# Kernel tuning notes

Hardware: AMD Instinct MI355X
Metric: run time of the kernel (lower is better)

The kernel has to match this reference:

```python
import math
import jax, jax.numpy as jnp
import numpy as np

IN_CH = 64
NUM_ANCHOR = 4
MAP_H, MAP_W = 96, 96
BATCH = 8
BN_EPS = 1e-5


def _conv2d(x, w, b, padding, dilation):
    # x: [B,C,H,W], w: [O,I,kh,kw] (OIHW)
    y = jax.lax.conv_general_dilated(
        x, w, window_strides=(1, 1),
        padding=((padding, padding), (padding, padding)),
        rhs_dilation=(dilation, dilation),
        dimension_numbers=('NCHW', 'OIHW', 'NCHW'))
    return y + b[None, :, None, None]


def _bn(x, gamma, beta, mean, var):
    scale = gamma / jnp.sqrt(var + BN_EPS)
    return x * scale[None, :, None, None] + (beta - mean * scale)[None, :, None, None]


def setup_inputs() -> dict:
    key = jax.random.key(0)
    ks = jax.random.split(key, 12)
    # cyclic channel-shift permutation matrices, one per anchor pass
    eye = np.eye(IN_CH, dtype=np.float32)
    shift = IN_CH // (2 * NUM_ANCHOR)
    perms = np.stack([eye[np.roll(np.arange(IN_CH), i * shift)] for i in range(2 * NUM_ANCHOR)])
    w_std = 1.0 / math.sqrt(IN_CH * 9)
    return {
        'x': jax.random.normal(ks[0], (BATCH, IN_CH, MAP_H, MAP_W), dtype=jnp.float32),
        'perms': jnp.asarray(perms),
        'dcn_w': jax.random.normal(ks[1], (IN_CH, IN_CH, 3, 3), dtype=jnp.float32) * w_std,
        'dcn_b': jax.random.normal(ks[2], (IN_CH,), dtype=jnp.float32) * 0.01,
        'conv2_w': jax.random.normal(ks[3], (IN_CH, IN_CH, 3, 3), dtype=jnp.float32) * w_std,
        'conv2_b': jax.random.normal(ks[4], (IN_CH,), dtype=jnp.float32) * 0.01,
        'conv3_w': jax.random.normal(ks[5], (IN_CH, IN_CH, 3, 3), dtype=jnp.float32) * w_std,
        'conv3_b': jax.random.normal(ks[6], (IN_CH,), dtype=jnp.float32) * 0.01,
        'bn_gamma': jax.random.uniform(ks[7], (3, IN_CH), dtype=jnp.float32, minval=0.5, maxval=1.5),
        'bn_beta': jax.random.normal(ks[8], (3, IN_CH), dtype=jnp.float32) * 0.1,
        'bn_mean': jax.random.normal(ks[9], (3, IN_CH), dtype=jnp.float32) * 0.1,
        'bn_var': jax.random.uniform(ks[10], (3, IN_CH), dtype=jnp.float32, minval=0.5, maxval=1.5),
    }


def reference(x, perms, dcn_w, dcn_b, conv2_w, conv2_b, conv3_w, conv3_b,
              bn_gamma, bn_beta, bn_mean, bn_var):
    h = x.shape[2]
    pad = math.ceil(h / (2 ** 1.5 + 2))  # 20 for h=96

    def conv_stack(o):
        # DCN at init (zero offsets) == plain 3x3 conv, pad=1
        o = jax.nn.relu(_bn(_conv2d(o, dcn_w, dcn_b, 1, 1), bn_gamma[0], bn_beta[0], bn_mean[0], bn_var[0]))
        o = jax.nn.relu(_bn(_conv2d(o, conv2_w, conv2_b, 2, 2), bn_gamma[1], bn_beta[1], bn_mean[1], bn_var[1]))
        o = jax.nn.relu(_bn(_conv2d(o, conv3_w, conv3_b, 2, 2), bn_gamma[2], bn_beta[2], bn_mean[2], bn_var[2]))
        return o

    outs = []
    for i in range(2 * NUM_ANCHOR):  # fixed small structural loop
        o = jnp.einsum('mn,bnhw->bmhw', perms[i], x)  # channel permutation
        if i % 2 != 0:
            o = jnp.pad(o, ((0, 0), (0, 0), (pad, pad), (pad, pad)))
        o = jnp.rot90(o, k=i % 4, axes=(-2, -1))   # ccw rotate
        o = conv_stack(o)
        o = jnp.rot90(o, k=(-i) % 4, axes=(-2, -1))  # cw rotate back
        if i % 2 != 0:
            H, W = o.shape[-2], o.shape[-1]
            sh, sw = (H - MAP_H) // 2, (W - MAP_W) // 2
            o = o[..., sh:sh + MAP_H, sw:sw + MAP_W]  # center crop
        outs.append(o)
    out_tensor = jnp.concatenate(outs, axis=1)  # [B, 8*C, H, W]
    out = jnp.max(out_tensor, axis=1, keepdims=True)
    # branch_name == 'midpoint', orientational_anchor=False -> clamped sigmoid
    return jnp.clip(jax.nn.sigmoid(out), 1e-4, 1.0 - 1e-4)
```

## Files before the change

kernel.cpp:

```cpp
#include <hip/hip_runtime.h>
#include <math.h>

#define B 8
#define C 64
#define HW 96
#define NWV 36864

typedef __attribute__((ext_vector_type(8)))  short short8;
typedef __attribute__((ext_vector_type(16))) float floatx16;

__device__ __forceinline__ unsigned short f2bf(float f) {
    unsigned int u = __float_as_uint(f);
    unsigned int r = (u + 0x7fffu + ((u >> 16) & 1u)) >> 16;
    return (unsigned short)r;
}

__device__ __forceinline__ void rotmap(int k, int ta, int tb, int& sa, int& sb) {
    switch (k) {
        case 0: sa = ta;     sb = tb;     break;
        case 1: sa = 2 - tb; sb = ta;     break;
        case 2: sa = 2 - ta; sb = 2 - tb; break;
        default: sa = tb;    sb = 2 - ta; break;
    }
}

__global__ void prep_w(const float* __restrict__ dcn_w, const float* __restrict__ c2w,
                       const float* __restrict__ c3w,
                       const float* __restrict__ gamma, const float* __restrict__ var_,
                       unsigned short* __restrict__ Wall) {
    int idx = blockIdx.x * 256 + threadIdx.x;
    if (idx >= 16 * NWV) return;
    int v = idx / NWV, rem = idx % NWV;
    int tap  = rem >> 12;
    int w12  = rem & 4095;
    int ks   = w12 >> 10;
    int cf   = (w12 >> 9) & 1;
    int lane = (w12 >> 3) & 63;
    int j    = w12 & 7;
    int co = cf * 32 + (lane & 31);
    int ci = ks * 16 + (lane >> 5) * 8 + j;
    int ta = tap / 3, tb = tap % 3;
    const float* src; int k, srcci, l;
    if (v < 8)       { k = v & 3;  srcci = (ci + 8 * v) & 63; src = dcn_w; l = 0; }
    else if (v < 12) { k = v - 8;  srcci = ci; src = c2w; l = 1; }
    else             { k = v - 12; srcci = ci; src = c3w; l = 2; }
    int sa, sb; rotmap(k, ta, tb, sa, sb);
    float s = gamma[l * 64 + co] * rsqrtf(var_[l * 64 + co] + 1e-5f);
    Wall[idx] = f2bf(src[((co * 64 + srcci) * 3 + sa) * 3 + sb] * s);
}

__global__ void prep_bias(const float* __restrict__ dcn_b, const float* __restrict__ c2b,
                          const float* __restrict__ c3b,
                          const float* __restrict__ gamma, const float* __restrict__ beta,
                          const float* __restrict__ mean, const float* __restrict__ var_,
                          float* __restrict__ biasg) {
    int t = threadIdx.x;
    if (t < 192) {
        int l = t >> 6, c = t & 63;
        const float* cb = (l == 0) ? dcn_b : ((l == 1) ? c2b : c3b);
        float s = gamma[l * 64 + c] * rsqrtf(var_[l * 64 + c] + 1e-5f);
        biasg[t] = cb[c] * s + beta[l * 64 + c] - mean[l * 64 + c] * s;
    }
}

__global__ __launch_bounds__(256) void prep_x(const float* __restrict__ in,
                                              unsigned short* __restrict__ out) {
    __shared__ float row[64 * 97];
    int by = blockIdx.x;
    int b = by / 96, y = by % 96;
    int t = threadIdx.x;
    for (int e = t; e < 6144; e += 256) {
        int c = e / 96, x = e - c * 96;
        row[c * 97 + x] = in[(((size_t)(b * 64 + c) * 96 + y) * 96) + x];
    }
    __syncthreads();
    for (int e = t; e < 6144; e += 256) {
        int x = e >> 6, c = e & 63;
        out[(((size_t)(b * 96 + y) * 96 + x) << 6) + c] = f2bf(row[c * 97 + x]);
    }
}

__global__ __launch_bounds__(256) void border_clear(unsigned short* __restrict__ buf1) {
    int idx = blockIdx.y;
    int br = (idx >> 3) * 2, b = idx & 7;
    int z = br * 8 + b;
    int i = blockIdx.x * 32 + (threadIdx.x >> 3);
    int g = threadIdx.x & 7;
    int r, c;
    if (i < 416)      { r = i / 104;              c = i % 104; }
    else if (i < 832) { int j = i - 416; r = 100 + j / 104; c = j % 104; }
    else              { int j = i - 832; r = 4 + (j >> 3); int c8 = j & 7;
                        c = (c8 < 4) ? c8 : 92 + c8; }
    uint4 zero = make_uint4(0u, 0u, 0u, 0u);
    *(uint4*)(buf1 + (size_t)z * (104 * 104 * 64) + ((size_t)(r * 104 + c) << 6) + (g << 3)) = zero;
}

__global__ __launch_bounds__(256, 2) void conv1_k(
    const unsigned short* __restrict__ xhwc, unsigned short* __restrict__ buf1,
    const unsigned short* __restrict__ Wall, const float* __restrict__ biasg) {

    __shared__ __align__(16) unsigned short xt[10 * 34 * 64];

    int z = blockIdx.z, br = z >> 3, b = z & 7, odd = br & 1;
    int fy0 = blockIdx.y * 8, fx0 = blockIdx.x * 32;
    int t = threadIdx.x, lane = t & 63, wv = t >> 6;
    int n = lane & 31, kq = lane >> 5;

    const unsigned short* xb = xhwc + ((size_t)b * 96 * 96 << 6);
    const short8* Ag = (const short8*)(Wall + (size_t)br * NWV);

    for (int e = t; e < 2720; e += 256) {
        int p = e >> 3, g = e & 7;
        int yy = p / 34, xx = p - yy * 34;
        int gy = fy0 - 5 + yy, gx = fx0 - 5 + xx;
        uint4 v = make_uint4(0u, 0u, 0u, 0u);
        if ((unsigned)gy < 96u && (unsigned)gx < 96u)
            v = *(const uint4*)(xb + ((size_t)(gy * 96 + gx) << 6) + (g << 3));
        *(uint4*)(xt + (p << 6) + ((g ^ (xx & 7)) << 3)) = v;
    }
    __syncthreads();

    floatx16 acc[2][2];
#pragma unroll
    for (int cf = 0; cf < 2; cf++)
#pragma unroll
        for (int pf = 0; pf < 2; pf++)
#pragma unroll
            for (int i = 0; i < 16; i++) acc[cf][pf][i] = 0.f;

#pragma unroll
    for (int ks = 0; ks < 4; ks++) {
#pragma unroll
        for (int tb = 0; tb < 3; tb++) {
            short8 a[3][2];
#pragma unroll
            for (int ta = 0; ta < 3; ta++)
#pragma unroll
                for (int cf = 0; cf < 2; cf++)
                    a[ta][cf] = Ag[(((ta * 3 + tb) * 4 + ks) * 2 + cf) * 64 + lane];
            int xx = n + tb;
            int g = ((ks * 2 + kq) ^ (xx & 7)) << 3;
            short8 bf[4];
#pragma unroll
            for (int rr = 0; rr < 4; rr++) {
                int p = (2 * wv + rr) * 34 + xx;
                bf[rr] = *(const short8*)(xt + (p << 6) + g);
            }
#pragma unroll
            for (int ta = 0; ta < 3; ta++)
#pragma unroll
                for (int pf = 0; pf < 2; pf++) {
                    int rr = pf + ta;
                    acc[0][pf] = __builtin_amdgcn_mfma_f32_32x32x16_bf16(a[ta][0], bf[rr], acc[0][pf], 0, 0, 0);
                    acc[1][pf] = __builtin_amdgcn_mfma_f32_32x32x16_bf16(a[ta][1], bf[rr], acc[1][pf], 0, 0, 0);
                }
        }
    }

    float4 bv[2][4];
#pragma unroll
    for (int cf = 0; cf < 2; cf++)
#pragma unroll
        for (int rb = 0; rb < 4; rb++)
            bv[cf][rb] = *(const float4*)(biasg + 32 * cf + 8 * rb + 4 * kq);

    __syncthreads();
#pragma unroll
    for (int pf = 0; pf < 2; pf++) {
        int pq = (2 * wv + pf) * 32 + n;
        int key = (pq & 7) << 1;
#pragma unroll
        for (int cf = 0; cf < 2; cf++)
#pragma unroll
            for (int rb = 0; rb < 4; rb++) {
                int u = kq + 2 * rb + 8 * cf;
                float v0 = fmaxf(acc[cf][pf][rb * 4 + 0] + bv[cf][rb].x, 0.f);
                float v1 = fmaxf(acc[cf][pf][rb * 4 + 1] + bv[cf][rb].y, 0.f);
                float v2 = fmaxf(acc[cf][pf][rb * 4 + 2] + bv[cf][rb].z, 0.f);
                float v3 = fmaxf(acc[cf][pf][rb * 4 + 3] + bv[cf][rb].w, 0.f);
                uint2 pk = make_uint2((unsigned)f2bf(v0) | ((unsigned)f2bf(v1) << 16),
                                      (unsigned)f2bf(v2) | ((unsigned)f2bf(v3) << 16));
                *(uint2*)((char*)xt + pq * 128 + ((u ^ key) << 3)) = pk;
            }
    }
    __syncthreads();

    unsigned short* fb = buf1 + (size_t)z * (104 * 104 * 64);
    int lo = odd ? 0 : 4, hi = odd ? 104 : 100;
    for (int e = t; e < 2048; e += 256) {
        int px = e >> 3, g = e & 7;
        int key = (px & 7) << 1;
        uint4 v = *(const uint4*)((const char*)xt + px * 128 + (((2 * g) ^ key) << 3));
        int lr = px >> 5, nn = px & 31;
        int f = fy0 + lr, fc = fx0 + nn;
        if (f >= lo && f < hi && fc >= lo && fc < hi)
            *(uint4*)(fb + ((size_t)(f * 104 + fc) << 6) + (g << 3)) = v;
    }
}

__global__ __launch_bounds__(512, 2) void conv23_k(
    const unsigned short* __restrict__ buf1, float* __restrict__ maxb,
    const unsigned short* __restrict__ Wall, const float* __restrict__ biasg) {

    __shared__ __align__(16) unsigned short c2out[768 * 64];
    __shared__ __align__(16) unsigned short xs[960 * 32];

    int z = blockIdx.z, br = z >> 3, odd = br & 1;
    int oy0 = blockIdx.y * 16, ox0 = blockIdx.x * 32;
    int t = threadIdx.x, lane = t & 63, wv = t >> 6;
    int n = lane & 31, kq = lane >> 5;

    const unsigned short* fb = buf1 + (size_t)z * (104 * 104 * 64);
    const short8* A2 = (const short8*)(Wall + (size_t)(8  + (br & 3)) * NWV);
    const short8* A3 = (const short8*)(Wall + (size_t)(12 + (br & 3)) * NWV);

    for (int e = t; e < 3840; e += 512) {
        int p = e >> 2, g = e & 3;
        int yy = p / 40, xx = p - yy * 40;
        uint4 v = *(const uint4*)(fb + ((size_t)((oy0 + yy) * 104 + ox0 + xx) << 6) + (g << 3));
        *(uint4*)(xs + (p << 5) + ((g ^ (xx & 3)) << 3)) = v;
    }
    __syncthreads();

    uint4 pfv[8];
#pragma unroll
    for (int k = 0; k < 8; k++) {
        int e = t + k * 512;
        if (e < 3840) {
            int p = e >> 2, g = e & 3;
            int yy = p / 40, xx = p - yy * 40;
            pfv[k] = *(const uint4*)(fb + ((size_t)((oy0 + yy) * 104 + ox0 + xx) << 6) + 32 + (g << 3));
        }
    }

    int q_[3], row2_[3], col2_[3];
#pragma unroll
    for (int jj = 0; jj < 3; jj++) {
        int q = 96 * wv + 32 * jj + n;
        q_[jj] = q;
        int qc = (q < 720) ? q : 719;
        int r2 = qc / 36;
        row2_[jj] = r2;
        col2_[jj] = qc - 36 * r2;
    }

    floatx16 acc2[3][2];
#pragma unroll
    for (int jj = 0; jj < 3; jj++)
#pragma unroll
        for (int cf = 0; cf < 2; cf++)
#pragma unroll
            for (int i = 0; i < 16; i++) acc2[jj][cf][i] = 0.f;

#pragma unroll
    for (int s = 0; s < 2; s++) {
        if (s == 1) {
            __syncthreads();
#pragma unroll
            for (int k = 0; k < 8; k++) {
                int e = t + k * 512;
                if (e < 3840) {
                    int p = e >> 2, g = e & 3;
                    int xx2 = p - (p / 40) * 40;
                    *(uint4*)(xs + (p << 5) + ((g ^ (xx2 & 3)) << 3)) = pfv[k];
                }
            }
            __syncthreads();
        }
#pragma unroll
        for (int kl = 0; kl < 2; kl++) {
            int ks = s * 2 + kl;
#pragma unroll
            for (int tb = 0; tb < 3; tb++) {
                short8 a[3][2];
#pragma unroll
                for (int ta = 0; ta < 3; ta++)
#pragma unroll
                    for (int cf = 0; cf < 2; cf++)
                        a[ta][cf] = A2[(((ta * 3 + tb) * 4 + ks) * 2 + cf) * 64 + lane];
#pragma unroll
                for (int jj = 0; jj < 3; jj++) {
                    int colx = col2_[jj] + 2 * tb;
                    int gsw = ((kl * 2 + kq) ^ (colx & 3)) << 3;
#pragma unroll
                    for (int ta = 0; ta < 3; ta++) {
                        int p = (row2_[jj] + 2 * ta) * 40 + colx;
                        short8 bfr = *(const short8*)(xs + (p << 5) + gsw);
                        acc2[jj][0] = __builtin_amdgcn_mfma_f32_32x32x16_bf16(a[ta][0], bfr, acc2[jj][0], 0, 0, 0);
                        acc2[jj][1] = __builtin_amdgcn_mfma_f32_32x32x16_bf16(a[ta][1], bfr, acc2[jj][1], 0, 0, 0);
                    }
                }
            }
        }
    }

    int rlo2 = (!odd && oy0 == 0)  ? 2  : 0;
    int rhi2 = (!odd && oy0 == 80) ? 18 : 20;
    int clo2 = (!odd && ox0 == 0)  ? 2  : 0;
    int chi2 = (!odd && ox0 == 64) ? 34 : 36;
    float4 bv2[2][4];
#pragma unroll
    for (int cf = 0; cf < 2; cf++)
#pragma unroll
        for (int rb = 0; rb < 4; rb++)
            bv2[cf][rb] = *(const float4*)(biasg + 64 + 32 * cf + 8 * rb + 4 * kq);

#pragma unroll
    for (int jj = 0; jj < 3; jj++) {
        if (q_[jj] < 720) {
            bool valid = (row2_[jj] >= rlo2) && (row2_[jj] < rhi2) &&
                         (col2_[jj] >= clo2) && (col2_[jj] < chi2);
            int key = col2_[jj] & 14;
#pragma unroll
            for (int cf = 0; cf < 2; cf++)
#pragma unroll
                for (int rb = 0; rb < 4; rb++) {
                    int u = kq + 2 * rb + 8 * cf;
                    float v0 = 0.f, v1 = 0.f, v2 = 0.f, v3 = 0.f;
                    if (valid) {
                        v0 = fmaxf(acc2[jj][cf][rb * 4 + 0] + bv2[cf][rb].x, 0.f);
                        v1 = fmaxf(acc2[jj][cf][rb * 4 + 1] + bv2[cf][rb].y, 0.f);
                        v2 = fmaxf(acc2[jj][cf][rb * 4 + 2] + bv2[cf][rb].z, 0.f);
                        v3 = fmaxf(acc2[jj][cf][rb * 4 + 3] + bv2[cf][rb].w, 0.f);
                    }
                    uint2 pk = make_uint2((unsigned)f2bf(v0) | ((unsigned)f2bf(v1) << 16),
                                          (unsigned)f2bf(v2) | ((unsigned)f2bf(v3) << 16));
                    *(uint2*)((char*)c2out + q_[jj] * 128 + ((u ^ key) << 3)) = pk;
                }
        }
    }
    __syncthreads();

    int r0 = 2 * wv;
    floatx16 acc3[2][2];
#pragma unroll
    for (int cf = 0; cf < 2; cf++)
#pragma unroll
        for (int pf = 0; pf < 2; pf++)
#pragma unroll
            for (int i = 0; i < 16; i++) acc3[cf][pf][i] = 0.f;

#pragma unroll
    for (int ks = 0; ks < 4; ks++) {
#pragma unroll
        for (int tb = 0; tb < 3; tb++) {
            short8 a[3][2];
#pragma unroll
            for (int ta = 0; ta < 3; ta++)
#pragma unroll
                for (int cf = 0; cf < 2; cf++)
                    a[ta][cf] = A3[(((ta * 3 + tb) * 4 + ks) * 2 + cf) * 64 + lane];
            int col = n + 2 * tb;
            int key = col & 14;
            int ublk = 2 * (ks * 2 + kq);
            short8 bf[6];
#pragma unroll
            for (int rr = 0; rr < 6; rr++) {
                int q = (r0 + rr) * 36 + col;
                bf[rr] = *(const short8*)((const char*)c2out + q * 128 + ((ublk ^ key) << 3));
            }
#pragma unroll
            for (int ta = 0; ta < 3; ta++)
#pragma unroll
                for (int pf = 0; pf < 2; pf++) {
                    int rr = pf + 2 * ta;
                    acc3[0][pf] = __builtin_amdgcn_mfma_f32_32x32x16_bf16(a[ta][0], bf[rr], acc3[0][pf], 0, 0, 0);
                    acc3[1][pf] = __builtin_amdgcn_mfma_f32_32x32x16_bf16(a[ta][1], bf[rr], acc3[1][pf], 0, 0, 0);
                }
        }
    }

    float4 bv3[2][4];
#pragma unroll
    for (int cf = 0; cf < 2; cf++)
#pragma unroll
        for (int rb = 0; rb < 4; rb++)
            bv3[cf][rb] = *(const float4*)(biasg + 128 + 32 * cf + 8 * rb + 4 * kq);

#pragma unroll
    for (int pf = 0; pf < 2; pf++) {
        float m = 0.f;
#pragma unroll
        for (int cf = 0; cf < 2; cf++)
#pragma unroll
            for (int rb = 0; rb < 4; rb++) {
                m = fmaxf(m, acc3[cf][pf][rb * 4 + 0] + bv3[cf][rb].x);
                m = fmaxf(m, acc3[cf][pf][rb * 4 + 1] + bv3[cf][rb].y);
                m = fmaxf(m, acc3[cf][pf][rb * 4 + 2] + bv3[cf][rb].z);
                m = fmaxf(m, acc3[cf][pf][rb * 4 + 3] + bv3[cf][rb].w);
            }
        m = fmaxf(m, 0.f);
        m = fmaxf(m, __shfl_xor(m, 32, 64));
        if (lane < 32)
            maxb[((size_t)z * 96 + oy0 + r0 + pf) * 96 + ox0 + n] = m;
    }
}

__global__ void final_k(const float* __restrict__ maxb, float* __restrict__ out) {
    int i = blockIdx.x * 256 + threadIdx.x;
    if (i < B * HW * HW) {
        int b = i / 9216, yx = i - b * 9216;
        float m = 0.f;
#pragma unroll
        for (int br = 0; br < 8; br++)
            m = fmaxf(m, maxb[((size_t)(br * 8 + b)) * 9216 + yx]);
        float v = 1.f / (1.f + expf(-m));
        out[i] = fminf(fmaxf(v, 1e-4f), 1.f - 1e-4f);
    }
}


extern "C" void kernel_launch(void* const* d_in, const int* in_sizes, int n_in,
                              void* d_out, int out_size, void* d_ws, size_t ws_size,
                              hipStream_t stream) {
    const float* x     = (const float*)d_in[0];
    const float* dcn_w = (const float*)d_in[2];
    const float* dcn_b = (const float*)d_in[3];
    const float* c2w   = (const float*)d_in[4];
    const float* c2b   = (const float*)d_in[5];
    const float* c3w   = (const float*)d_in[6];
    const float* c3b   = (const float*)d_in[7];
    const float* gamma = (const float*)d_in[8];
    const float* beta  = (const float*)d_in[9];
    const float* mean  = (const float*)d_in[10];
    const float* var_  = (const float*)d_in[11];

    char* ws = (char*)d_ws;
    unsigned short* Wall = (unsigned short*)ws;
    size_t off = (size_t)16 * NWV * 2;
    float* biasg = (float*)(ws + off);            off += 1024;
    float* maxb  = (float*)(ws + off);            off += (size_t)64 * 9216 * 4;
    unsigned short* xhwc = (unsigned short*)(ws + off); off += (size_t)B * 9216 * 64 * 2;
    unsigned short* buf1 = (unsigned short*)(ws + off);

    prep_w<<<(16 * NWV + 255) / 256, 256, 0, stream>>>(dcn_w, c2w, c3w, gamma, var_, Wall);
    prep_bias<<<1, 256, 0, stream>>>(dcn_b, c2b, c3b, gamma, beta, mean, var_, biasg);
    prep_x<<<B * 96, 256, 0, stream>>>(x, xhwc);
    border_clear<<<dim3(50, 32), 256, 0, stream>>>(buf1);

    dim3 g1(4, 13, 64);
    conv1_k<<<g1, 256, 0, stream>>>(xhwc, buf1, Wall, biasg);

    dim3 g23(3, 6, 64);
    conv23_k<<<g23, 512, 0, stream>>>(buf1, maxb, Wall, biasg);

    final_k<<<(B * HW * HW + 255) / 256, 256, 0, stream>>>(maxb, (float*)d_out);
}
```

Before: 310.5 us.

## Make conv23 persistent over 256 blocks with cross-tile prefetch

Replaces the 1152-block conv23 grid with 256 persistent blocks, each looping over a contiguous range of tiles. While conv3 runs on the current tile, the block prefetches the first channel half of the next tile's input into registers and writes it to shared memory afterwards. Bias loads are hoisted out of the loop. This hides global load latency and removes tail-wave imbalance, but adds register pressure and leaves 4-5 tiles per block, which may lower occupancy.

```diff
diff --git a/kernel.cpp b/kernel.cpp
--- a/kernel.cpp
+++ b/kernel.cpp
@@ -205,33 +205,20 @@
     __shared__ __align__(16) unsigned short c2out[768 * 64];
     __shared__ __align__(16) unsigned short xs[960 * 32];
 
-    int z = blockIdx.z, br = z >> 3, odd = br & 1;
-    int oy0 = blockIdx.y * 16, ox0 = blockIdx.x * 32;
     int t = threadIdx.x, lane = t & 63, wv = t >> 6;
     int n = lane & 31, kq = lane >> 5;
 
-    const unsigned short* fb = buf1 + (size_t)z * (104 * 104 * 64);
-    const short8* A2 = (const short8*)(Wall + (size_t)(8  + (br & 3)) * NWV);
-    const short8* A3 = (const short8*)(Wall + (size_t)(12 + (br & 3)) * NWV);
-
-    for (int e = t; e < 3840; e += 512) {
-        int p = e >> 2, g = e & 3;
-        int yy = p / 40, xx = p - yy * 40;
-        uint4 v = *(const uint4*)(fb + ((size_t)((oy0 + yy) * 104 + ox0 + xx) << 6) + (g << 3));
-        *(uint4*)(xs + (p << 5) + ((g ^ (xx & 3)) << 3)) = v;
-    }
-    __syncthreads();
-
-    uint4 pfv[8];
-#pragma unroll
-    for (int k = 0; k < 8; k++) {
-        int e = t + k * 512;
-        if (e < 3840) {
-            int p = e >> 2, g = e & 3;
-            int yy = p / 40, xx = p - yy * 40;
-            pfv[k] = *(const uint4*)(fb + ((size_t)((oy0 + yy) * 104 + ox0 + xx) << 6) + 32 + (g << 3));
-        }
-    }
+    int i0 = (blockIdx.x * 1152) >> 8;
+    int i1 = ((blockIdx.x + 1) * 1152) >> 8;
+
+    float4 bv2[2][4], bv3[2][4];
+#pragma unroll
+    for (int cf = 0; cf < 2; cf++)
+#pragma unroll
+        for (int rb = 0; rb < 4; rb++) {
+            bv2[cf][rb] = *(const float4*)(biasg + 64  + 32 * cf + 8 * rb + 4 * kq);
+            bv3[cf][rb] = *(const float4*)(biasg + 128 + 32 * cf + 8 * rb + 4 * kq);
+        }
 
     int q_[3], row2_[3], col2_[3];
 #pragma unroll
@@ -244,155 +231,206 @@
         col2_[jj] = qc - 36 * r2;
     }
 
-    floatx16 acc2[3][2];
-#pragma unroll
-    for (int jj = 0; jj < 3; jj++)
+    {
+        int z = i0 / 18, r = i0 - z * 18;
+        int oy0 = (r % 6) * 16, ox0 = (r / 6) * 32;
+        const unsigned short* fb = buf1 + (size_t)z * (104 * 104 * 64);
+        for (int e = t; e < 3840; e += 512) {
+            int p = e >> 2, g = e & 3;
+            int yy = p / 40, xx = p - yy * 40;
+            uint4 v = *(const uint4*)(fb + ((size_t)((oy0 + yy) * 104 + ox0 + xx) << 6) + (g << 3));
+            *(uint4*)(xs + (p << 5) + ((g ^ (xx & 3)) << 3)) = v;
+        }
+    }
+
+    for (int i = i0; i < i1; ++i) {
+        int z = i / 18, r = i - z * 18;
+        int br = z >> 3, odd = br & 1;
+        int oy0 = (r % 6) * 16, ox0 = (r / 6) * 32;
+        const unsigned short* fb = buf1 + (size_t)z * (104 * 104 * 64);
+        const short8* A2 = (const short8*)(Wall + (size_t)(8  + (br & 3)) * NWV);
+        const short8* A3 = (const short8*)(Wall + (size_t)(12 + (br & 3)) * NWV);
+
+        __syncthreads();
+
+        uint4 pfv[8];
+#pragma unroll
+        for (int k = 0; k < 8; k++) {
+            int e = t + k * 512;
+            if (e < 3840) {
+                int p = e >> 2, g = e & 3;
+                int yy = p / 40, xx = p - yy * 40;
+                pfv[k] = *(const uint4*)(fb + ((size_t)((oy0 + yy) * 104 + ox0 + xx) << 6) + 32 + (g << 3));
+            }
+        }
+
+        floatx16 acc2[3][2];
+#pragma unroll
+        for (int jj = 0; jj < 3; jj++)
+#pragma unroll
+            for (int cf = 0; cf < 2; cf++)
+#pragma unroll
+                for (int q = 0; q < 16; q++) acc2[jj][cf][q] = 0.f;
+
+#pragma unroll
+        for (int s = 0; s < 2; s++) {
+            if (s == 1) {
+                __syncthreads();
+#pragma unroll
+                for (int k = 0; k < 8; k++) {
+                    int e = t + k * 512;
+                    if (e < 3840) {
+                        int p = e >> 2, g = e & 3;
+                        int xx2 = p - (p / 40) * 40;
+                        *(uint4*)(xs + (p << 5) + ((g ^ (xx2 & 3)) << 3)) = pfv[k];
+                    }
+                }
+                __syncthreads();
+            }
+#pragma unroll
+            for (int kl = 0; kl < 2; kl++) {
+                int ks = s * 2 + kl;
+#pragma unroll
+                for (int tb = 0; tb < 3; tb++) {
+                    short8 a[3][2];
+#pragma unroll
+                    for (int ta = 0; ta < 3; ta++)
+#pragma unroll
+                        for (int cf = 0; cf < 2; cf++)
+                            a[ta][cf] = A2[(((ta * 3 + tb) * 4 + ks) * 2 + cf) * 64 + lane];
+#pragma unroll
+                    for (int jj = 0; jj < 3; jj++) {
+                        int colx = col2_[jj] + 2 * tb;
+                        int gsw = ((kl * 2 + kq) ^ (colx & 3)) << 3;
+#pragma unroll
+                        for (int ta = 0; ta < 3; ta++) {
+                            int p = (row2_[jj] + 2 * ta) * 40 + colx;
+                            short8 bfr = *(const short8*)(xs + (p << 5) + gsw);
+                            acc2[jj][0] = __builtin_amdgcn_mfma_f32_32x32x16_bf16(a[ta][0], bfr, acc2[jj][0], 0, 0, 0);
+                            acc2[jj][1] = __builtin_amdgcn_mfma_f32_32x32x16_bf16(a[ta][1], bfr, acc2[jj][1], 0, 0, 0);
+                        }
+                    }
+                }
+            }
+        }
+
+        int rlo2 = (!odd && oy0 == 0)  ? 2  : 0;
+        int rhi2 = (!odd && oy0 == 80) ? 18 : 20;
+        int clo2 = (!odd && ox0 == 0)  ? 2  : 0;
+        int chi2 = (!odd && ox0 == 64) ? 34 : 36;
+
+#pragma unroll
+        for (int jj = 0; jj < 3; jj++) {
+            if (q_[jj] < 720) {
+                bool valid = (row2_[jj] >= rlo2) && (row2_[jj] < rhi2) &&
+                             (col2_[jj] >= clo2) && (col2_[jj] < chi2);
+                int key = col2_[jj] & 14;
+#pragma unroll
+                for (int cf = 0; cf < 2; cf++)
+#pragma unroll
+                    for (int rb = 0; rb < 4; rb++) {
+                        int u = kq + 2 * rb + 8 * cf;
+                        float v0 = 0.f, v1 = 0.f, v2 = 0.f, v3 = 0.f;
+                        if (valid) {
+                            v0 = fmaxf(acc2[jj][cf][rb * 4 + 0] + bv2[cf][rb].x, 0.f);
+                            v1 = fmaxf(acc2[jj][cf][rb * 4 + 1] + bv2[cf][rb].y, 0.f);
+                            v2 = fmaxf(acc2[jj][cf][rb * 4 + 2] + bv2[cf][rb].z, 0.f);
+                            v3 = fmaxf(acc2[jj][cf][rb * 4 + 3] + bv2[cf][rb].w, 0.f);
+                        }
+                        uint2 pk = make_uint2((unsigned)f2bf(v0) | ((unsigned)f2bf(v1) << 16),
+                                              (unsigned)f2bf(v2) | ((unsigned)f2bf(v3) << 16));
+                        *(uint2*)((char*)c2out + q_[jj] * 128 + ((u ^ key) << 3)) = pk;
+                    }
+            }
+        }
+        __syncthreads();
+
+        bool have_next = (i + 1 < i1);
+        uint4 nfv[8];
+        if (have_next) {
+            int ni = i + 1;
+            int nz = ni / 18, nr = ni - nz * 18;
+            int noy0 = (nr % 6) * 16, nox0 = (nr / 6) * 32;
+            const unsigned short* nfb = buf1 + (size_t)nz * (104 * 104 * 64);
+#pragma unroll
+            for (int k = 0; k < 8; k++) {
+                int e = t + k * 512;
+                if (e < 3840) {
+                    int p = e >> 2, g = e & 3;
+                    int yy = p / 40, xx = p - yy * 40;
+                    nfv[k] = *(const uint4*)(nfb + ((size_t)((noy0 + yy) * 104 + nox0 + xx) << 6) + (g << 3));
+                }
+            }
+        }
+
+        int r0 = 2 * wv;
+        floatx16 acc3[2][2];
 #pragma unroll
         for (int cf = 0; cf < 2; cf++)
 #pragma unroll
-            for (int i = 0; i < 16; i++) acc2[jj][cf][i] = 0.f;
-
-#pragma unroll
-    for (int s = 0; s < 2; s++) {
-        if (s == 1) {
-            __syncthreads();
+            for (int pf = 0; pf < 2; pf++)
+#pragma unroll
+                for (int q = 0; q < 16; q++) acc3[cf][pf][q] = 0.f;
+
+#pragma unroll
+        for (int ks = 0; ks < 4; ks++) {
+#pragma unroll
+            for (int tb = 0; tb < 3; tb++) {
+                short8 a[3][2];
+#pragma unroll
+                for (int ta = 0; ta < 3; ta++)
+#pragma unroll
+                    for (int cf = 0; cf < 2; cf++)
+                        a[ta][cf] = A3[(((ta * 3 + tb) * 4 + ks) * 2 + cf) * 64 + lane];
+                int col = n + 2 * tb;
+                int key = col & 14;
+                int ublk = 2 * (ks * 2 + kq);
+                short8 bf[6];
+#pragma unroll
+                for (int rr = 0; rr < 6; rr++) {
+                    int q = (r0 + rr) * 36 + col;
+                    bf[rr] = *(const short8*)((const char*)c2out + q * 128 + ((ublk ^ key) << 3));
+                }
+#pragma unroll
+                for (int ta = 0; ta < 3; ta++)
+#pragma unroll
+                    for (int pf = 0; pf < 2; pf++) {
+                        int rr = pf + 2 * ta;
+                        acc3[0][pf] = __builtin_amdgcn_mfma_f32_32x32x16_bf16(a[ta][0], bf[rr], acc3[0][pf], 0, 0, 0);
+                        acc3[1][pf] = __builtin_amdgcn_mfma_f32_32x32x16_bf16(a[ta][1], bf[rr], acc3[1][pf], 0, 0, 0);
+                    }
+            }
+        }
+
+        if (have_next) {
 #pragma unroll
             for (int k = 0; k < 8; k++) {
                 int e = t + k * 512;
                 if (e < 3840) {
                     int p = e >> 2, g = e & 3;
                     int xx2 = p - (p / 40) * 40;
-                    *(uint4*)(xs + (p << 5) + ((g ^ (xx2 & 3)) << 3)) = pfv[k];
-                }
-            }
-            __syncthreads();
-        }
-#pragma unroll
-        for (int kl = 0; kl < 2; kl++) {
-            int ks = s * 2 + kl;
-#pragma unroll
-            for (int tb = 0; tb < 3; tb++) {
-                short8 a[3][2];
-#pragma unroll
-                for (int ta = 0; ta < 3; ta++)
-#pragma unroll
-                    for (int cf = 0; cf < 2; cf++)
-                        a[ta][cf] = A2[(((ta * 3 + tb) * 4 + ks) * 2 + cf) * 64 + lane];
-#pragma unroll
-                for (int jj = 0; jj < 3; jj++) {
-                    int colx = col2_[jj] + 2 * tb;
-                    int gsw = ((kl * 2 + kq) ^ (colx & 3)) << 3;
-#pragma unroll
-                    for (int ta = 0; ta < 3; ta++) {
-                        int p = (row2_[jj] + 2 * ta) * 40 + colx;
-                        short8 bfr = *(const short8*)(xs + (p << 5) + gsw);
-                        acc2[jj][0] = __builtin_amdgcn_mfma_f32_32x32x16_bf16(a[ta][0], bfr, acc2[jj][0], 0, 0, 0);
-                        acc2[jj][1] = __builtin_amdgcn_mfma_f32_32x32x16_bf16(a[ta][1], bfr, acc2[jj][1], 0, 0, 0);
-                    }
-                }
-            }
-        }
-    }
-
-    int rlo2 = (!odd && oy0 == 0)  ? 2  : 0;
-    int rhi2 = (!odd && oy0 == 80) ? 18 : 20;
-    int clo2 = (!odd && ox0 == 0)  ? 2  : 0;
-    int chi2 = (!odd && ox0 == 64) ? 34 : 36;
-    float4 bv2[2][4];
-#pragma unroll
-    for (int cf = 0; cf < 2; cf++)
-#pragma unroll
-        for (int rb = 0; rb < 4; rb++)
-            bv2[cf][rb] = *(const float4*)(biasg + 64 + 32 * cf + 8 * rb + 4 * kq);
-
-#pragma unroll
-    for (int jj = 0; jj < 3; jj++) {
-        if (q_[jj] < 720) {
-            bool valid = (row2_[jj] >= rlo2) && (row2_[jj] < rhi2) &&
-                         (col2_[jj] >= clo2) && (col2_[jj] < chi2);
-            int key = col2_[jj] & 14;
+                    *(uint4*)(xs + (p << 5) + ((g ^ (xx2 & 3)) << 3)) = nfv[k];
+                }
+            }
+        }
+
+#pragma unroll
+        for (int pf = 0; pf < 2; pf++) {
+            float m = 0.f;
 #pragma unroll
             for (int cf = 0; cf < 2; cf++)
 #pragma unroll
                 for (int rb = 0; rb < 4; rb++) {
-                    int u = kq + 2 * rb + 8 * cf;
-                    float v0 = 0.f, v1 = 0.f, v2 = 0.f, v3 = 0.f;
-                    if (valid) {
-                        v0 = fmaxf(acc2[jj][cf][rb * 4 + 0] + bv2[cf][rb].x, 0.f);
-                        v1 = fmaxf(acc2[jj][cf][rb * 4 + 1] + bv2[cf][rb].y, 0.f);
-                        v2 = fmaxf(acc2[jj][cf][rb * 4 + 2] + bv2[cf][rb].z, 0.f);
-                        v3 = fmaxf(acc2[jj][cf][rb * 4 + 3] + bv2[cf][rb].w, 0.f);
-                    }
-                    uint2 pk = make_uint2((unsigned)f2bf(v0) | ((unsigned)f2bf(v1) << 16),
-                                          (unsigned)f2bf(v2) | ((unsigned)f2bf(v3) << 16));
-                    *(uint2*)((char*)c2out + q_[jj] * 128 + ((u ^ key) << 3)) = pk;
-                }
-        }
-    }
-    __syncthreads();
-
-    int r0 = 2 * wv;
-    floatx16 acc3[2][2];
-#pragma unroll
-    for (int cf = 0; cf < 2; cf++)
-#pragma unroll
-        for (int pf = 0; pf < 2; pf++)
-#pragma unroll
-            for (int i = 0; i < 16; i++) acc3[cf][pf][i] = 0.f;
-
-#pragma unroll
-    for (int ks = 0; ks < 4; ks++) {
-#pragma unroll
-        for (int tb = 0; tb < 3; tb++) {
-            short8 a[3][2];
-#pragma unroll
-            for (int ta = 0; ta < 3; ta++)
-#pragma unroll
-                for (int cf = 0; cf < 2; cf++)
-                    a[ta][cf] = A3[(((ta * 3 + tb) * 4 + ks) * 2 + cf) * 64 + lane];
-            int col = n + 2 * tb;
-            int key = col & 14;
-            int ublk = 2 * (ks * 2 + kq);
-            short8 bf[6];
-#pragma unroll
-            for (int rr = 0; rr < 6; rr++) {
-                int q = (r0 + rr) * 36 + col;
-                bf[rr] = *(const short8*)((const char*)c2out + q * 128 + ((ublk ^ key) << 3));
-            }
-#pragma unroll
-            for (int ta = 0; ta < 3; ta++)
-#pragma unroll
-                for (int pf = 0; pf < 2; pf++) {
-                    int rr = pf + 2 * ta;
-                    acc3[0][pf] = __builtin_amdgcn_mfma_f32_32x32x16_bf16(a[ta][0], bf[rr], acc3[0][pf], 0, 0, 0);
-                    acc3[1][pf] = __builtin_amdgcn_mfma_f32_32x32x16_bf16(a[ta][1], bf[rr], acc3[1][pf], 0, 0, 0);
-                }
-        }
-    }
-
-    float4 bv3[2][4];
-#pragma unroll
-    for (int cf = 0; cf < 2; cf++)
-#pragma unroll
-        for (int rb = 0; rb < 4; rb++)
-            bv3[cf][rb] = *(const float4*)(biasg + 128 + 32 * cf + 8 * rb + 4 * kq);
-
-#pragma unroll
-    for (int pf = 0; pf < 2; pf++) {
-        float m = 0.f;
-#pragma unroll
-        for (int cf = 0; cf < 2; cf++)
-#pragma unroll
-            for (int rb = 0; rb < 4; rb++) {
-                m = fmaxf(m, acc3[cf][pf][rb * 4 + 0] + bv3[cf][rb].x);
-                m = fmaxf(m, acc3[cf][pf][rb * 4 + 1] + bv3[cf][rb].y);
-                m = fmaxf(m, acc3[cf][pf][rb * 4 + 2] + bv3[cf][rb].z);
-                m = fmaxf(m, acc3[cf][pf][rb * 4 + 3] + bv3[cf][rb].w);
-            }
-        m = fmaxf(m, 0.f);
-        m = fmaxf(m, __shfl_xor(m, 32, 64));
-        if (lane < 32)
-            maxb[((size_t)z * 96 + oy0 + r0 + pf) * 96 + ox0 + n] = m;
+                    m = fmaxf(m, acc3[cf][pf][rb * 4 + 0] + bv3[cf][rb].x);
+                    m = fmaxf(m, acc3[cf][pf][rb * 4 + 1] + bv3[cf][rb].y);
+                    m = fmaxf(m, acc3[cf][pf][rb * 4 + 2] + bv3[cf][rb].z);
+                    m = fmaxf(m, acc3[cf][pf][rb * 4 + 3] + bv3[cf][rb].w);
+                }
+            m = fmaxf(m, 0.f);
+            m = fmaxf(m, __shfl_xor(m, 32, 64));
+            if (lane < 32)
+                maxb[((size_t)z * 96 + oy0 + r0 + pf) * 96 + ox0 + n] = m;
+        }
     }
 }
 
@@ -441,8 +479,7 @@
     dim3 g1(4, 13, 64);
     conv1_k<<<g1, 256, 0, stream>>>(xhwc, buf1, Wall, biasg);
 
-    dim3 g23(3, 6, 64);
-    conv23_k<<<g23, 512, 0, stream>>>(buf1, maxb, Wall, biasg);
+    conv23_k<<<dim3(256), 512, 0, stream>>>(buf1, maxb, Wall, biasg);
 
     final_k<<<(B * HW * HW + 255) / 256, 256, 0, stream>>>(maxb, (float*)d_out);
 }
```

Result: slower. 527.5 us (+69.9%).
